# Kernel optimization log

Measured on AMD Instinct MI355X. Metric: run time of the kernel, lower is better.

## Reference

```python
import math
import jax, jax.numpy as jnp
import numpy as np

B, N, D = 32, 1025, 768        # batch, tokens (incl. CLS), backbone channels
C, CD, TD = 64, 128, 256       # num_clusters, cluster_dim, token_dim
REG = 0.1
SINKHORN_ITERS = 5


def setup_inputs() -> dict:
    key = jax.random.key(0)
    ks = jax.random.split(key, 9)
    inv = 1.0 / math.sqrt(D)
    return {
        "x": jax.random.normal(ks[0], (B, N, D), dtype=jnp.float32),
        "Wf": jax.random.normal(ks[1], (D, CD), dtype=jnp.float32) * inv,
        "bf": jnp.zeros((CD,), dtype=jnp.float32),
        "Ws": jax.random.normal(ks[2], (D, C), dtype=jnp.float32) * inv,
        "bs": jnp.zeros((C,), dtype=jnp.float32),
        "Wt": jax.random.normal(ks[3], (D, TD), dtype=jnp.float32) * inv,
        "bt": jnp.zeros((TD,), dtype=jnp.float32),
        "anchors": jax.random.normal(ks[4], (C, CD), dtype=jnp.float32) * 0.1,
        "dust_bin": jnp.array(1.0, dtype=jnp.float32),
        "sharpness": jnp.array(5.0, dtype=jnp.float32),
    }


def _sinkhorn_log(log_a, log_b, M, num_iters, reg):
    # log-domain Sinkhorn: M [B, C+1, Nt], log_a [B, C+1], log_b [B, Nt]
    M = M / reg
    u = jnp.zeros_like(log_a)
    v = jnp.zeros_like(log_b)
    for _ in range(num_iters):
        u = log_a - jax.nn.logsumexp(M + v[:, None, :], axis=2)
        v = log_b - jax.nn.logsumexp(M + u[:, :, None], axis=1)
    return M + u[:, :, None] + v[:, None, :]


def reference(x, Wf, bf, Ws, bs, Wt, bt, anchors, dust_bin, sharpness):
    Bx, Nx, _ = x.shape
    n_tok = Nx - 1
    nC = anchors.shape[0]

    t_global = x[:, 0]            # [B, D]
    fi = x[:, 1:]                 # [B, Nt, D]

    f = fi @ Wf + bf              # [B, Nt, CD]
    s = jnp.einsum('bnd,dc->bcn', fi, Ws) + bs[None, :, None]  # [B, C, Nt]
    s = s * sharpness

    dust = jnp.broadcast_to(dust_bin, (Bx, 1, n_tok))
    s_aug = jnp.concatenate([s, dust], axis=1)  # [B, C+1, Nt]

    log_b = jnp.full((Bx, n_tok), -math.log(n_tok), dtype=x.dtype)
    # n_tok (1024) > nC (64): marginals with dustbin absorbing excess mass
    log_a = jnp.concatenate([
        jnp.full((Bx, nC), -math.log(n_tok), dtype=x.dtype),
        jnp.full((Bx, 1), math.log(n_tok - nC) - math.log(n_tok), dtype=x.dtype),
    ], axis=1)

    log_P = _sinkhorn_log(log_a, log_b, s_aug, SINKHORN_ITERS, REG)
    p = jnp.exp(log_P)[:, :-1, :]  # [B, C, Nt], drop dustbin row

    # sum_n p[b,c,n] * (2*f[b,n,d] - anchors[c,d])  == GEMM + rank-1 correction
    v_agg = 2.0 * jnp.einsum('bcn,bnd->bcd', p, f) \
            - p.sum(axis=2)[:, :, None] * anchors[None]  # [B, C, CD]

    v_local = v_agg.reshape(Bx, -1)   # [B, C*CD]
    v_global = t_global @ Wt + bt     # [B, TD]
    f_out = jnp.concatenate([v_global, v_local], axis=-1)
    norm = jnp.maximum(jnp.linalg.norm(f_out, axis=-1, keepdims=True), 1e-12)
    return f_out / norm
```

## Files before the change

### kernel.cpp

```cpp
#include <hip/hip_runtime.h>

typedef unsigned short u16;
typedef __attribute__((ext_vector_type(8))) short bf16x8;
typedef __attribute__((ext_vector_type(8))) short s16x8;
typedef __attribute__((ext_vector_type(4))) float f32x4;
typedef __attribute__((ext_vector_type(4))) short s16x4;

#define OUTW 8448

static __device__ __forceinline__ float bf2f(u16 u) {
    union { unsigned int i; float f; } x; x.i = ((unsigned int)u) << 16; return x.f;
}
static __device__ __forceinline__ u16 f2bf(float f) {
    union { float f; unsigned int i; } x; x.f = f;
    unsigned int lsb = (x.i >> 16) & 1u;
    return (u16)((x.i + 0x7fffu + lsb) >> 16);
}
static __device__ __forceinline__ int kswz(int r, int c) {
    return c ^ (((r ^ (r >> 3)) & 7) << 3);
}

__global__ __launch_bounds__(256) void k_pre(
    const float* __restrict__ x, const float* __restrict__ Wf, const float* __restrict__ Ws,
    const float* __restrict__ Wt, u16* __restrict__ Bp, float* __restrict__ vg)
{
    const int bid = blockIdx.x, tid = threadIdx.x;
    if (bid < 12) {
        __shared__ float Wl[64][193];
        const int t = bid;
        #pragma unroll 4
        for (int i = 0; i < 32; ++i) {
            const int idx = i * 256 + tid, r = idx >> 7, c = idx & 127;
            Wl[r][c] = Wf[(size_t)(t * 64 + r) * 128 + c];
        }
        #pragma unroll 4
        for (int i = 0; i < 16; ++i) {
            const int idx = i * 256 + tid, r = idx >> 6, c = idx & 63;
            Wl[r][128 + c] = Ws[(size_t)(t * 64 + r) * 64 + c];
        }
        __syncthreads();
        #pragma unroll
        for (int i = 0; i < 6; ++i) {
            const int ch = i * 256 + tid, c = ch >> 3, j0 = (ch & 7) << 3;
            u16 pk[8];
            #pragma unroll
            for (int j = 0; j < 8; ++j) pk[j] = f2bf(Wl[j0 + j][c]);
            *(s16x8*)&Bp[((size_t)t * 192 + c) * 64 + j0] = *(const s16x8*)pk;
        }
    } else {
        const int blk = bid - 12;
        const int kc = blk >> 5, b = blk & 31, d = tid;
        const float* xr = x + (size_t)b * (1025 * 768) + kc * 96;
        const float* wp = Wt + (size_t)kc * 96 * 256 + d;
        float acc = 0.f;
        #pragma unroll 8
        for (int k = 0; k < 96; ++k) acc += xr[k] * wp[(size_t)k * 256];
        vg[(size_t)blk * 256 + d] = acc;
    }
}

__global__ __launch_bounds__(256, 4) void k_gemm1(
    const float* __restrict__ x, const u16* __restrict__ Bp,
    const float* __restrict__ bf_, const float* __restrict__ bs_, const float* __restrict__ sharp,
    u16* __restrict__ fT, float* __restrict__ sM)
{
    __shared__ u16 Asm[2][32][72];
    const int tid  = threadIdx.x;
    const int lane = tid & 63;
    const int w    = tid >> 6;
    const int b    = blockIdx.x >> 5;
    const int n0   = (blockIdx.x & 31) << 5;
    const float* Abase = x + ((size_t)b * 1025 + 1 + n0) * 768;

    const int arow = tid >> 3, ak0 = (tid & 7) << 3;
    const float* aptr = Abase + (size_t)arow * 768 + ak0;
    const int fk = (lane >> 4) << 3;
    const u16* bbase = Bp + (size_t)(w * 48 + (lane & 15)) * 64 + fk;

    f32x4 acc[2][3] = {};
    float4 pa[2];
    bf16x8 bcur[6], bnxt[6];

    pa[0] = *(const float4*)(aptr);
    pa[1] = *(const float4*)(aptr + 4);
    #pragma unroll
    for (int nt = 0; nt < 3; ++nt)
        #pragma unroll
        for (int kk = 0; kk < 2; ++kk)
            bcur[nt * 2 + kk] = *(const bf16x8*)(bbase + nt * 1024 + kk * 32);
    {
        u16 t8[8];
        t8[0] = f2bf(pa[0].x); t8[1] = f2bf(pa[0].y); t8[2] = f2bf(pa[0].z); t8[3] = f2bf(pa[0].w);
        t8[4] = f2bf(pa[1].x); t8[5] = f2bf(pa[1].y); t8[6] = f2bf(pa[1].z); t8[7] = f2bf(pa[1].w);
        *(s16x8*)&Asm[0][arow][ak0] = *(const s16x8*)t8;
    }
    pa[0] = *(const float4*)(aptr + 64);
    pa[1] = *(const float4*)(aptr + 68);
    __syncthreads();

    for (int t = 0; t < 12; ++t) {
        const int cur = t & 1;
        if (t < 11) {
            const u16* bp1 = bbase + (size_t)(t + 1) * 12288;
            #pragma unroll
            for (int nt = 0; nt < 3; ++nt)
                #pragma unroll
                for (int kk = 0; kk < 2; ++kk)
                    bnxt[nt * 2 + kk] = *(const bf16x8*)(bp1 + nt * 1024 + kk * 32);
            u16 t8[8];
            t8[0] = f2bf(pa[0].x); t8[1] = f2bf(pa[0].y); t8[2] = f2bf(pa[0].z); t8[3] = f2bf(pa[0].w);
            t8[4] = f2bf(pa[1].x); t8[5] = f2bf(pa[1].y); t8[6] = f2bf(pa[1].z); t8[7] = f2bf(pa[1].w);
            *(s16x8*)&Asm[cur ^ 1][arow][ak0] = *(const s16x8*)t8;
        }
        if (t < 10) {
            const float* ap = aptr + (size_t)(t + 2) * 64;
            pa[0] = *(const float4*)(ap);
            pa[1] = *(const float4*)(ap + 4);
        }
        #pragma unroll
        for (int kk = 0; kk < 2; ++kk) {
            bf16x8 af[2];
            af[0] = *(const bf16x8*)&Asm[cur][(lane & 15)][kk * 32 + fk];
            af[1] = *(const bf16x8*)&Asm[cur][16 + (lane & 15)][kk * 32 + fk];
            #pragma unroll
            for (int nt = 0; nt < 3; ++nt) {
                acc[0][nt] = __builtin_amdgcn_mfma_f32_16x16x32_bf16(af[0], bcur[nt * 2 + kk], acc[0][nt], 0, 0, 0);
                acc[1][nt] = __builtin_amdgcn_mfma_f32_16x16x32_bf16(af[1], bcur[nt * 2 + kk], acc[1][nt], 0, 0, 0);
            }
        }
        if (t < 11) {
            #pragma unroll
            for (int i = 0; i < 6; ++i) bcur[i] = bnxt[i];
        }
        __syncthreads();
    }

    const int rbase = (lane >> 4) << 2;
    const int cl = lane & 15;
    const float sc = sharp[0] * 10.0f;
    #pragma unroll
    for (int mt = 0; mt < 2; ++mt) {
        const int nbase = n0 + mt * 16 + rbase;
        #pragma unroll
        for (int nt = 0; nt < 3; ++nt) {
            const int col16 = w * 48 + nt * 16;
            const int c = col16 + cl;
            if (col16 < 128) {
                const float bias = bf_[c];
                u16 pk[4];
                #pragma unroll
                for (int r = 0; r < 4; ++r) pk[r] = f2bf(acc[mt][nt][r] + bias);
                *(s16x4*)&fT[((size_t)b * 128 + c) * 1024 + nbase] = *(const s16x4*)pk;
            } else {
                const int cm = c - 128;
                const float bias = bs_[cm];
                float4 v;
                v.x = (acc[mt][nt][0] + bias) * sc;
                v.y = (acc[mt][nt][1] + bias) * sc;
                v.z = (acc[mt][nt][2] + bias) * sc;
                v.w = (acc[mt][nt][3] + bias) * sc;
                *(float4*)&sM[((size_t)b * 64 + cm) * 1024 + nbase] = v;
            }
        }
    }
}

__global__ __launch_bounds__(1024, 1) void k_tail(
    const float* __restrict__ sM, const u16* __restrict__ fT,
    const float* __restrict__ vg, const float* __restrict__ bt,
    const float* __restrict__ anchors, float* __restrict__ out)
{
    __shared__ u16   Ksm[64][1024];
    __shared__ float betas[1024];
    __shared__ float alph[68];
    __shared__ float rsL[64];
    __shared__ float sred[16];
    const int b = blockIdx.x, tid = threadIdx.x, l = tid & 63, w = tid >> 6;
    const float* Mb = sM + (size_t)b * 64 * 1024;

    #pragma unroll
    for (int i = 0; i < 4; ++i) {
        const int c = w * 4 + i;
        float v[16];
        #pragma unroll
        for (int q = 0; q < 4; ++q)
            *(float4*)(v + q * 4) = *(const float4*)(Mb + (size_t)c * 1024 + l * 16 + q * 4);
        float mx = v[0];
        #pragma unroll
        for (int j = 1; j < 16; ++j) mx = fmaxf(mx, v[j]);
        #pragma unroll
        for (int off = 32; off > 0; off >>= 1) mx = fmaxf(mx, __shfl_xor(mx, off));
        u16 e[16];
        #pragma unroll
        for (int j = 0; j < 16; ++j) e[j] = f2bf(__expf(v[j] - mx));
        *(s16x8*)&Ksm[c][kswz(c, l * 16)]     = *(const s16x8*)(e);
        *(s16x8*)&Ksm[c][kswz(c, l * 16 + 8)] = *(const s16x8*)(e + 8);
    }
    betas[tid] = 1.0f;
    __syncthreads();

    const float a_c = 1.0f / 1024.0f, a_dust = 960.0f / 1024.0f, b_n = 1.0f / 1024.0f;
    const int r8  = (l & 7) * 8;
    const int cg  = w * 8 + (l >> 3);
    const int bwi = (cg & 63) + ((cg >> 6) << 9);

    for (int it = 0; it < 5; ++it) {
        float bb[16];
        #pragma unroll
        for (int j = 0; j < 2; ++j)
            #pragma unroll
            for (int m = 0; m < 8; ++m)
                bb[j * 8 + m] = betas[l + m * 64 + j * 512];
        float sb = 0.f;
        #pragma unroll
        for (int j = 0; j < 16; ++j) sb += bb[j];
        #pragma unroll
        for (int off = 32; off > 0; off >>= 1) sb += __shfl_xor(sb, off);
        #pragma unroll
        for (int i = 0; i < 4; ++i) {
            const int c = w * 4 + i;
            float s = 0.f;
            #pragma unroll
            for (int j = 0; j < 2; ++j) {
                const bf16x8 kr = *(const bf16x8*)&Ksm[c][kswz(c, 8 * l + 512 * j)];
                #pragma unroll
                for (int m = 0; m < 8; ++m) s += bf2f((u16)kr[m]) * bb[j * 8 + m];
            }
            #pragma unroll
            for (int off = 32; off > 0; off >>= 1) s += __shfl_xor(s, off);
            if (l == 0) alph[c] = a_c / s;
        }
        if (tid == 0) alph[64] = a_dust / sb;
        __syncthreads();
        f32x4 a0 = *(const f32x4*)&alph[r8];
        f32x4 a1 = *(const f32x4*)&alph[r8 + 4];
        const float ad = alph[64];
        float sc8[8] = {};
        #pragma unroll
        for (int i = 0; i < 8; ++i) {
            const bf16x8 kb = *(const bf16x8*)&Ksm[r8 + i][kswz(r8 + i, cg * 8)];
            const float av = (i < 4) ? a0[i] : a1[i - 4];
            #pragma unroll
            for (int m = 0; m < 8; ++m) sc8[m] += bf2f((u16)kb[m]) * av;
        }
        #pragma unroll
        for (int off = 1; off < 8; off <<= 1)
            #pragma unroll
            for (int m = 0; m < 8; ++m) sc8[m] += __shfl_xor(sc8[m], off);
        if ((l & 7) == 0) {
            #pragma unroll
            for (int m = 0; m < 8; ++m) betas[bwi + m * 64] = b_n / (sc8[m] + ad);
        }
        __syncthreads();
    }

    {
        float bb[16];
        #pragma unroll
        for (int j = 0; j < 2; ++j)
            #pragma unroll
            for (int m = 0; m < 8; ++m)
                bb[j * 8 + m] = betas[l + m * 64 + j * 512];
        #pragma unroll
        for (int i = 0; i < 4; ++i) {
            const int c = w * 4 + i;
            const float ac = alph[c];
            float s = 0.f;
            u16 pk[16];
            #pragma unroll
            for (int j = 0; j < 2; ++j) {
                const bf16x8 kr = *(const bf16x8*)&Ksm[c][kswz(c, 8 * l + 512 * j)];
                #pragma unroll
                for (int m = 0; m < 8; ++m) {
                    const float tv = bf2f((u16)kr[m]) * bb[j * 8 + m];
                    s += tv;
                    pk[j * 8 + m] = f2bf(ac * tv);
                }
            }
            #pragma unroll
            for (int off = 32; off > 0; off >>= 1) s += __shfl_xor(s, off);
            if (l == 0) rsL[c] = ac * s;
            *(s16x8*)&Ksm[c][kswz(c, 8 * l)]       = *(const s16x8*)(pk);
            *(s16x8*)&Ksm[c][kswz(c, 8 * l + 512)] = *(const s16x8*)(pk + 8);
        }
    }
    __syncthreads();

    const int wng = w & 7, wmt = w >> 3;
    const int fk = (l >> 4) << 3;
    const int ar0 = wmt * 32 + (l & 15);
    const int ar1 = ar0 + 16;
    const u16* brow = fT + ((size_t)b * 128 + wng * 16 + (l & 15)) * 1024 + fk;
    f32x4 acc2[2] = {};
    #pragma unroll 4
    for (int ks = 0; ks < 32; ++ks) {
        const bf16x8 a0 = *(const bf16x8*)&Ksm[ar0][kswz(ar0, ks * 32 + fk)];
        const bf16x8 a1 = *(const bf16x8*)&Ksm[ar1][kswz(ar1, ks * 32 + fk)];
        const bf16x8 b0 = *(const bf16x8*)(brow + ks * 32);
        acc2[0] = __builtin_amdgcn_mfma_f32_16x16x32_bf16(a0, b0, acc2[0], 0, 0, 0);
        acc2[1] = __builtin_amdgcn_mfma_f32_16x16x32_bf16(a1, b0, acc2[1], 0, 0, 0);
    }

    float vgv = 0.f, ss = 0.f;
    if (tid < 256) {
        float v = bt[tid];
        #pragma unroll
        for (int kc = 0; kc < 8; ++kc) v += vg[(size_t)(kc * 32 + b) * 256 + tid];
        vgv = v; ss = v * v;
    }
    const int d5 = wng * 16 + (l & 15);
    float vloc[2][4];
    #pragma unroll
    for (int mt = 0; mt < 2; ++mt) {
        #pragma unroll
        for (int r = 0; r < 4; ++r) {
            const int c = wmt * 32 + mt * 16 + ((l >> 4) << 2) + r;
            const float vv = 2.0f * acc2[mt][r] - rsL[c] * anchors[c * 128 + d5];
            vloc[mt][r] = vv; ss += vv * vv;
        }
    }
    #pragma unroll
    for (int off = 32; off > 0; off >>= 1) ss += __shfl_xor(ss, off);
    if (l == 0) sred[w] = ss;
    __syncthreads();
    float tot = 0.f;
    #pragma unroll
    for (int i = 0; i < 16; ++i) tot += sred[i];
    const float inv = 1.0f / fmaxf(sqrtf(tot), 1e-12f);
    if (tid < 256) out[(size_t)b * OUTW + tid] = vgv * inv;
    #pragma unroll
    for (int mt = 0; mt < 2; ++mt) {
        #pragma unroll
        for (int r = 0; r < 4; ++r) {
            const int c = wmt * 32 + mt * 16 + ((l >> 4) << 2) + r;
            out[(size_t)b * OUTW + 256 + (size_t)c * 128 + d5] = vloc[mt][r] * inv;
        }
    }
}

extern "C" void kernel_launch(void* const* d_in, const int* in_sizes, int n_in,
                              void* d_out, int out_size, void* d_ws, size_t ws_size,
                              hipStream_t stream)
{
    const float* x      = (const float*)d_in[0];
    const float* Wf     = (const float*)d_in[1];
    const float* bf_    = (const float*)d_in[2];
    const float* Ws     = (const float*)d_in[3];
    const float* bs_    = (const float*)d_in[4];
    const float* Wt     = (const float*)d_in[5];
    const float* bt     = (const float*)d_in[6];
    const float* anchors= (const float*)d_in[7];
    const float* sharp  = (const float*)d_in[9];

    char* ws = (char*)d_ws;
    u16*   fT = (u16*)(ws);
    float* sM = (float*)(ws + 8388608);
    u16*   Bp = (u16*)(ws + 16777216);
    float* vg = (float*)(ws + 17072128);
    float* out = (float*)d_out;

    k_pre  <<<dim3(268),  256,  0, stream>>>(x, Wf, Ws, Wt, Bp, vg);
    k_gemm1<<<dim3(1024), 256,  0, stream>>>(x, Bp, bf_, bs_, sharp, fT, sM);
    k_tail <<<dim3(32),   1024, 0, stream>>>(sM, fT, vg, bt, anchors, out);
}
```

Before: 246.0 us.

## Stage full A tile in LDS for gemm1 and split tail into sink, agg, norm kernels

The first GEMM now loads the whole 32x768 A slice into LDS once, converting it to bf16 up front. This replaces the double-buffered k-loop with its per-step barriers, and lowers the occupancy hint from 4 to 3 blocks. The single 32-block tail kernel is split into three kernels: Sinkhorn writes P and row sums to global memory, a 256-block aggregation GEMM writes unnormalized outputs plus partial sums of squares, and a normalization kernel rescales each row. The goal is to spread the aggregation GEMM across more CUs than one block per batch, at the cost of extra launches and a global round trip for P and the output.

```diff
diff --git a/kernel.cpp b/kernel.cpp
--- a/kernel.cpp
+++ b/kernel.cpp
@@ -59,12 +59,12 @@
     }
 }
 
-__global__ __launch_bounds__(256, 4) void k_gemm1(
+__global__ __launch_bounds__(256, 3) void k_gemm1(
     const float* __restrict__ x, const u16* __restrict__ Bp,
     const float* __restrict__ bf_, const float* __restrict__ bs_, const float* __restrict__ sharp,
     u16* __restrict__ fT, float* __restrict__ sM)
 {
-    __shared__ u16 Asm[2][32][72];
+    __shared__ u16 Asm[32][776];
     const int tid  = threadIdx.x;
     const int lane = tid & 63;
     const int w    = tid >> 6;
@@ -72,71 +72,44 @@
     const int n0   = (blockIdx.x & 31) << 5;
     const float* Abase = x + ((size_t)b * 1025 + 1 + n0) * 768;
 
-    const int arow = tid >> 3, ak0 = (tid & 7) << 3;
-    const float* aptr = Abase + (size_t)arow * 768 + ak0;
+    #pragma unroll
+    for (int j = 0; j < 24; ++j) {
+        const int slot = j * 256 + tid;
+        const int r = slot / 192, f4 = slot - r * 192;
+        const float4 v = *(const float4*)(Abase + (size_t)r * 768 + f4 * 4);
+        u16 pk[4];
+        pk[0] = f2bf(v.x); pk[1] = f2bf(v.y); pk[2] = f2bf(v.z); pk[3] = f2bf(v.w);
+        *(s16x4*)&Asm[r][f4 * 4] = *(const s16x4*)pk;
+    }
+    __syncthreads();
+
+    f32x4 acc[2][3] = {};
     const int fk = (lane >> 4) << 3;
-    const u16* bbase = Bp + (size_t)(w * 48 + (lane & 15)) * 64 + fk;
-
-    f32x4 acc[2][3] = {};
-    float4 pa[2];
-    bf16x8 bcur[6], bnxt[6];
-
-    pa[0] = *(const float4*)(aptr);
-    pa[1] = *(const float4*)(aptr + 4);
-    #pragma unroll
-    for (int nt = 0; nt < 3; ++nt)
-        #pragma unroll
-        for (int kk = 0; kk < 2; ++kk)
-            bcur[nt * 2 + kk] = *(const bf16x8*)(bbase + nt * 1024 + kk * 32);
-    {
-        u16 t8[8];
-        t8[0] = f2bf(pa[0].x); t8[1] = f2bf(pa[0].y); t8[2] = f2bf(pa[0].z); t8[3] = f2bf(pa[0].w);
-        t8[4] = f2bf(pa[1].x); t8[5] = f2bf(pa[1].y); t8[6] = f2bf(pa[1].z); t8[7] = f2bf(pa[1].w);
-        *(s16x8*)&Asm[0][arow][ak0] = *(const s16x8*)t8;
-    }
-    pa[0] = *(const float4*)(aptr + 64);
-    pa[1] = *(const float4*)(aptr + 68);
-    __syncthreads();
-
-    for (int t = 0; t < 12; ++t) {
-        const int cur = t & 1;
-        if (t < 11) {
-            const u16* bp1 = bbase + (size_t)(t + 1) * 12288;
-            #pragma unroll
-            for (int nt = 0; nt < 3; ++nt)
-                #pragma unroll
-                for (int kk = 0; kk < 2; ++kk)
-                    bnxt[nt * 2 + kk] = *(const bf16x8*)(bp1 + nt * 1024 + kk * 32);
-            u16 t8[8];
-            t8[0] = f2bf(pa[0].x); t8[1] = f2bf(pa[0].y); t8[2] = f2bf(pa[0].z); t8[3] = f2bf(pa[0].w);
-            t8[4] = f2bf(pa[1].x); t8[5] = f2bf(pa[1].y); t8[6] = f2bf(pa[1].z); t8[7] = f2bf(pa[1].w);
-            *(s16x8*)&Asm[cur ^ 1][arow][ak0] = *(const s16x8*)t8;
-        }
-        if (t < 10) {
-            const float* ap = aptr + (size_t)(t + 2) * 64;
-            pa[0] = *(const float4*)(ap);
-            pa[1] = *(const float4*)(ap + 4);
-        }
+    const int al = lane & 15;
+    const u16* bbase = Bp + (size_t)(w * 48 + al) * 64 + fk;
+    #pragma unroll 3
+    for (int ks = 0; ks < 12; ++ks) {
+        const u16* bp = bbase + (size_t)ks * 12288;
+        bf16x8 bfr[6];
+        #pragma unroll
+        for (int nt = 0; nt < 3; ++nt)
+            #pragma unroll
+            for (int kk = 0; kk < 2; ++kk)
+                bfr[nt * 2 + kk] = *(const bf16x8*)(bp + nt * 1024 + kk * 32);
         #pragma unroll
         for (int kk = 0; kk < 2; ++kk) {
-            bf16x8 af[2];
-            af[0] = *(const bf16x8*)&Asm[cur][(lane & 15)][kk * 32 + fk];
-            af[1] = *(const bf16x8*)&Asm[cur][16 + (lane & 15)][kk * 32 + fk];
+            const int kb = ks * 64 + kk * 32 + fk;
+            const bf16x8 af0 = *(const bf16x8*)&Asm[al][kb];
+            const bf16x8 af1 = *(const bf16x8*)&Asm[16 + al][kb];
             #pragma unroll
             for (int nt = 0; nt < 3; ++nt) {
-                acc[0][nt] = __builtin_amdgcn_mfma_f32_16x16x32_bf16(af[0], bcur[nt * 2 + kk], acc[0][nt], 0, 0, 0);
-                acc[1][nt] = __builtin_amdgcn_mfma_f32_16x16x32_bf16(af[1], bcur[nt * 2 + kk], acc[1][nt], 0, 0, 0);
+                acc[0][nt] = __builtin_amdgcn_mfma_f32_16x16x32_bf16(af0, bfr[nt * 2 + kk], acc[0][nt], 0, 0, 0);
+                acc[1][nt] = __builtin_amdgcn_mfma_f32_16x16x32_bf16(af1, bfr[nt * 2 + kk], acc[1][nt], 0, 0, 0);
             }
         }
-        if (t < 11) {
-            #pragma unroll
-            for (int i = 0; i < 6; ++i) bcur[i] = bnxt[i];
-        }
-        __syncthreads();
     }
 
     const int rbase = (lane >> 4) << 2;
-    const int cl = lane & 15;
     const float sc = sharp[0] * 10.0f;
     #pragma unroll
     for (int mt = 0; mt < 2; ++mt) {
@@ -144,7 +117,7 @@
         #pragma unroll
         for (int nt = 0; nt < 3; ++nt) {
             const int col16 = w * 48 + nt * 16;
-            const int c = col16 + cl;
+            const int c = col16 + al;
             if (col16 < 128) {
                 const float bias = bf_[c];
                 u16 pk[4];
@@ -165,16 +138,12 @@
     }
 }
 
-__global__ __launch_bounds__(1024, 1) void k_tail(
-    const float* __restrict__ sM, const u16* __restrict__ fT,
-    const float* __restrict__ vg, const float* __restrict__ bt,
-    const float* __restrict__ anchors, float* __restrict__ out)
+__global__ __launch_bounds__(1024, 1) void k_sink(
+    const float* __restrict__ sM, u16* __restrict__ p_out, float* __restrict__ rs_out)
 {
     __shared__ u16   Ksm[64][1024];
     __shared__ float betas[1024];
     __shared__ float alph[68];
-    __shared__ float rsL[64];
-    __shared__ float sred[16];
     const int b = blockIdx.x, tid = threadIdx.x, l = tid & 63, w = tid >> 6;
     const float* Mb = sM + (size_t)b * 64 * 1024;
 
@@ -254,87 +223,95 @@
         __syncthreads();
     }
 
-    {
-        float bb[16];
-        #pragma unroll
-        for (int j = 0; j < 2; ++j)
-            #pragma unroll
-            for (int m = 0; m < 8; ++m)
-                bb[j * 8 + m] = betas[l + m * 64 + j * 512];
-        #pragma unroll
-        for (int i = 0; i < 4; ++i) {
-            const int c = w * 4 + i;
-            const float ac = alph[c];
-            float s = 0.f;
-            u16 pk[16];
-            #pragma unroll
-            for (int j = 0; j < 2; ++j) {
-                const bf16x8 kr = *(const bf16x8*)&Ksm[c][kswz(c, 8 * l + 512 * j)];
-                #pragma unroll
-                for (int m = 0; m < 8; ++m) {
-                    const float tv = bf2f((u16)kr[m]) * bb[j * 8 + m];
-                    s += tv;
-                    pk[j * 8 + m] = f2bf(ac * tv);
-                }
+    float bb[16];
+    #pragma unroll
+    for (int j = 0; j < 2; ++j)
+        #pragma unroll
+        for (int m = 0; m < 8; ++m)
+            bb[j * 8 + m] = betas[l + m * 64 + j * 512];
+    #pragma unroll
+    for (int i = 0; i < 4; ++i) {
+        const int c = w * 4 + i;
+        const float ac = alph[c];
+        float s = 0.f;
+        u16 pk[16];
+        #pragma unroll
+        for (int j = 0; j < 2; ++j) {
+            const bf16x8 kr = *(const bf16x8*)&Ksm[c][kswz(c, 8 * l + 512 * j)];
+            #pragma unroll
+            for (int m = 0; m < 8; ++m) {
+                const float tv = bf2f((u16)kr[m]) * bb[j * 8 + m];
+                s += tv;
+                pk[j * 8 + m] = f2bf(ac * tv);
             }
-            #pragma unroll
-            for (int off = 32; off > 0; off >>= 1) s += __shfl_xor(s, off);
-            if (l == 0) rsL[c] = ac * s;
-            *(s16x8*)&Ksm[c][kswz(c, 8 * l)]       = *(const s16x8*)(pk);
-            *(s16x8*)&Ksm[c][kswz(c, 8 * l + 512)] = *(const s16x8*)(pk + 8);
-        }
-    }
+        }
+        #pragma unroll
+        for (int off = 32; off > 0; off >>= 1) s += __shfl_xor(s, off);
+        if (l == 0) rs_out[b * 64 + c] = ac * s;
+        u16* pg = p_out + ((size_t)b * 64 + c) * 1024 + 8 * l;
+        *(s16x8*)(pg)       = *(const s16x8*)(pk);
+        *(s16x8*)(pg + 512) = *(const s16x8*)(pk + 8);
+    }
+}
+
+__global__ __launch_bounds__(256) void k_agg(
+    const u16* __restrict__ p, const u16* __restrict__ fT,
+    const float* __restrict__ rs, const float* __restrict__ anchors,
+    float* __restrict__ out, float* __restrict__ ssp)
+{
+    const int b = blockIdx.x >> 3, dg = blockIdx.x & 7;
+    const int tid = threadIdx.x, l = tid & 63, w = tid >> 6;
+    const int fk = (l >> 4) << 3;
+    const u16* arow = p  + ((size_t)b * 64  + w * 16 + (l & 15)) * 1024 + fk;
+    const u16* brow = fT + ((size_t)b * 128 + dg * 16 + (l & 15)) * 1024 + fk;
+    f32x4 acc = {};
+    #pragma unroll 8
+    for (int ks = 0; ks < 32; ++ks) {
+        const bf16x8 a  = *(const bf16x8*)(arow + ks * 32);
+        const bf16x8 bb = *(const bf16x8*)(brow + ks * 32);
+        acc = __builtin_amdgcn_mfma_f32_16x16x32_bf16(a, bb, acc, 0, 0, 0);
+    }
+    const int d = dg * 16 + (l & 15);
+    float ssl = 0.f;
+    #pragma unroll
+    for (int r = 0; r < 4; ++r) {
+        const int c = w * 16 + ((l >> 4) << 2) + r;
+        const float vv = 2.0f * acc[r] - rs[b * 64 + c] * anchors[c * 128 + d];
+        out[(size_t)b * OUTW + 256 + (size_t)c * 128 + d] = vv;
+        ssl += vv * vv;
+    }
+    #pragma unroll
+    for (int off = 32; off > 0; off >>= 1) ssl += __shfl_xor(ssl, off);
+    __shared__ float part[4];
+    if (l == 0) part[w] = ssl;
     __syncthreads();
-
-    const int wng = w & 7, wmt = w >> 3;
-    const int fk = (l >> 4) << 3;
-    const int ar0 = wmt * 32 + (l & 15);
-    const int ar1 = ar0 + 16;
-    const u16* brow = fT + ((size_t)b * 128 + wng * 16 + (l & 15)) * 1024 + fk;
-    f32x4 acc2[2] = {};
-    #pragma unroll 4
-    for (int ks = 0; ks < 32; ++ks) {
-        const bf16x8 a0 = *(const bf16x8*)&Ksm[ar0][kswz(ar0, ks * 32 + fk)];
-        const bf16x8 a1 = *(const bf16x8*)&Ksm[ar1][kswz(ar1, ks * 32 + fk)];
-        const bf16x8 b0 = *(const bf16x8*)(brow + ks * 32);
-        acc2[0] = __builtin_amdgcn_mfma_f32_16x16x32_bf16(a0, b0, acc2[0], 0, 0, 0);
-        acc2[1] = __builtin_amdgcn_mfma_f32_16x16x32_bf16(a1, b0, acc2[1], 0, 0, 0);
-    }
-
-    float vgv = 0.f, ss = 0.f;
-    if (tid < 256) {
-        float v = bt[tid];
-        #pragma unroll
-        for (int kc = 0; kc < 8; ++kc) v += vg[(size_t)(kc * 32 + b) * 256 + tid];
-        vgv = v; ss = v * v;
-    }
-    const int d5 = wng * 16 + (l & 15);
-    float vloc[2][4];
-    #pragma unroll
-    for (int mt = 0; mt < 2; ++mt) {
-        #pragma unroll
-        for (int r = 0; r < 4; ++r) {
-            const int c = wmt * 32 + mt * 16 + ((l >> 4) << 2) + r;
-            const float vv = 2.0f * acc2[mt][r] - rsL[c] * anchors[c * 128 + d5];
-            vloc[mt][r] = vv; ss += vv * vv;
-        }
-    }
+    if (tid == 0) ssp[b * 8 + dg] = part[0] + part[1] + part[2] + part[3];
+}
+
+__global__ __launch_bounds__(256) void k_norm(
+    const float* __restrict__ vg, const float* __restrict__ bt,
+    const float* __restrict__ ssp, float* __restrict__ out)
+{
+    const int b = blockIdx.x, t = threadIdx.x;
+    float v = bt[t];
+    #pragma unroll
+    for (int kc = 0; kc < 8; ++kc) v += vg[(size_t)(kc * 32 + b) * 256 + t];
+    float ss = v * v;
     #pragma unroll
     for (int off = 32; off > 0; off >>= 1) ss += __shfl_xor(ss, off);
-    if (l == 0) sred[w] = ss;
+    __shared__ float part[4];
+    if ((t & 63) == 0) part[t >> 6] = ss;
     __syncthreads();
-    float tot = 0.f;
-    #pragma unroll
-    for (int i = 0; i < 16; ++i) tot += sred[i];
+    float tot = part[0] + part[1] + part[2] + part[3];
+    #pragma unroll
+    for (int i = 0; i < 8; ++i) tot += ssp[b * 8 + i];
     const float inv = 1.0f / fmaxf(sqrtf(tot), 1e-12f);
-    if (tid < 256) out[(size_t)b * OUTW + tid] = vgv * inv;
-    #pragma unroll
-    for (int mt = 0; mt < 2; ++mt) {
-        #pragma unroll
-        for (int r = 0; r < 4; ++r) {
-            const int c = wmt * 32 + mt * 16 + ((l >> 4) << 2) + r;
-            out[(size_t)b * OUTW + 256 + (size_t)c * 128 + d5] = vloc[mt][r] * inv;
-        }
+    out[(size_t)b * OUTW + t] = v * inv;
+    float* row = out + (size_t)b * OUTW + 256;
+    #pragma unroll 8
+    for (int j = 0; j < 32; ++j) {
+        const int idx = j * 256 + t;
+        row[idx] *= inv;
     }
 }
 
@@ -357,9 +334,14 @@
     float* sM = (float*)(ws + 8388608);
     u16*   Bp = (u16*)(ws + 16777216);
     float* vg = (float*)(ws + 17072128);
+    float* rs = (float*)(ws + 17334272);
+    u16*   p  = (u16*)(ws + 17342464);
+    float* ssp= (float*)(ws + 21536768);
     float* out = (float*)d_out;
 
     k_pre  <<<dim3(268),  256,  0, stream>>>(x, Wf, Ws, Wt, Bp, vg);
     k_gemm1<<<dim3(1024), 256,  0, stream>>>(x, Bp, bf_, bs_, sharp, fT, sM);
-    k_tail <<<dim3(32),   1024, 0, stream>>>(sM, fT, vg, bt, anchors, out);
-}
+    k_sink <<<dim3(32),   1024, 0, stream>>>(sM, p, rs);
+    k_agg  <<<dim3(256),  256,  0, stream>>>(p, fT, rs, anchors, out, ssp);
+    k_norm <<<dim3(32),   256,  0, stream>>>(vg, bt, ssp, out);
+}
```

Result: slower. 269.7 us (+9.6%).
